# Kernel tuning notes

Measured on AMD Instinct MI355X. Metric: run time of the kernel, lower is better.

Reference implementation:

```python
import jax, jax.numpy as jnp
import numpy as np

B, S, IN, OUT, E, K = 4, 2048, 4096, 4096, 8, 16
POOLS = E * K  # 128 rank-one pools


def setup_inputs() -> dict:
    key = jax.random.key(0)
    k1, k2, k3, k4, k5 = jax.random.split(key, 5)
    sc = 0.02
    return {
        "hidden_states": jax.random.normal(k1, (B, S, IN), jnp.float32),
        "w0": jax.random.normal(k2, (OUT, IN), jnp.float32) * sc,   # pretrained Linear weight
        "b0": jnp.zeros((OUT,), jnp.float32),                        # pretrained Linear bias
        "wr": jax.random.normal(k3, (POOLS, IN), jnp.float32) * sc,  # Router stacked v.T
        "u": jax.random.normal(k4, (OUT, POOLS), jnp.float32) * sc,  # RankOnePools.u
        "svh": jax.random.normal(k5, (POOLS, IN), jnp.float32) * sc, # RankOnePools.svh
        "top_k": 2,
    }


def reference(hidden_states, w0, b0, wr, u, svh, top_k):
    # pretrained dense path (expert_use_diff=True)
    pretrained_out = jnp.einsum('bsi,oi->bso', hidden_states, w0) + b0

    x = hidden_states.reshape(-1, hidden_states.shape[-1])  # [N, IN]

    # Router: logits over num_experts*k rank-one pools
    logits = jnp.einsum('ni,pi->np', x, wr)                  # [N, POOLS]
    vals, idx = jax.lax.top_k(logits, top_k)                 # [N, top_k]
    vals = vals / jnp.sum(vals, axis=-1, keepdims=True)      # computed but UNUSED (matches original torch code)

    # RankOnePools: gather selected rank-one factors and combine
    svh_sel = svh[idx]                                       # [N, top_k, IN]
    dot = jnp.einsum('ni,nti->nt', x, svh_sel)               # [N, top_k]
    u_sel = u.T[idx]                                         # [N, top_k, OUT]
    expert_out = jnp.einsum('nt,nto->no', dot, u_sel)        # [N, OUT]

    out = pretrained_out + expert_out.reshape(pretrained_out.shape)
    return out
```

## Files before the change

kernel.cpp:

```cpp
#include <hip/hip_runtime.h>

#define K_DIM  4096
#define N_OUT  4096
#define N_TOK  8192
#define N_POOL 128

typedef __bf16 bf16x8 __attribute__((ext_vector_type(8)));
typedef float  f32x4  __attribute__((ext_vector_type(4)));
typedef unsigned short u16x8 __attribute__((ext_vector_type(8)));

#define AS1 __attribute__((address_space(1)))
#define AS3 __attribute__((address_space(3)))

__device__ __forceinline__ unsigned short f2bf(float f) {
    union { float f; unsigned u; } v; v.f = f;
    unsigned r = v.u + 0x7fffu + ((v.u >> 16) & 1u);
    return (unsigned short)(r >> 16);
}
__device__ __forceinline__ float bf2f(unsigned short b) {
    union { unsigned u; float f; } v; v.u = ((unsigned)b) << 16;
    return v.f;
}

__global__ __launch_bounds__(256) void k_convert_w0(const float* __restrict__ w0,
                                                    unsigned short* __restrict__ w0b) {
    size_t base = ((size_t)blockIdx.x * 256 + threadIdx.x) * 8;
    float4 a = *(const float4*)(w0 + base);
    float4 b = *(const float4*)(w0 + base + 4);
    u16x8 r;
    r[0] = f2bf(a.x); r[1] = f2bf(a.y); r[2] = f2bf(a.z); r[3] = f2bf(a.w);
    r[4] = f2bf(b.x); r[5] = f2bf(b.y); r[6] = f2bf(b.z); r[7] = f2bf(b.w);
    *(u16x8*)(w0b + base) = r;
}

__global__ __launch_bounds__(256) void k_convert_x(const float* __restrict__ x,
                                                   unsigned short* __restrict__ xh) {
    size_t base = ((size_t)blockIdx.x * 256 + threadIdx.x) * 8;
    float4 a = *(const float4*)(x + base);
    float4 b = *(const float4*)(x + base + 4);
    u16x8 r;
    r[0] = f2bf(a.x); r[1] = f2bf(a.y); r[2] = f2bf(a.z); r[3] = f2bf(a.w);
    r[4] = f2bf(b.x); r[5] = f2bf(b.y); r[6] = f2bf(b.z); r[7] = f2bf(b.w);
    *(u16x8*)(xh + base) = r;
}

__global__ __launch_bounds__(256) void k_convert_wr(const float* __restrict__ wr,
                                                    unsigned short* __restrict__ wrh) {
    size_t base = ((size_t)blockIdx.x * 256 + threadIdx.x) * 8;
    float4 a = *(const float4*)(wr + base);
    float4 b = *(const float4*)(wr + base + 4);
    u16x8 r;
    r[0] = f2bf(a.x); r[1] = f2bf(a.y); r[2] = f2bf(a.z); r[3] = f2bf(a.w);
    r[4] = f2bf(b.x); r[5] = f2bf(b.y); r[6] = f2bf(b.z); r[7] = f2bf(b.w);
    *(u16x8*)(wrh + base) = r;
}

__global__ __launch_bounds__(256) void k_transpose_u(const float* __restrict__ u,
                                                     float* __restrict__ uT) {
    __shared__ float t[32][65];
    const int o0 = blockIdx.x * 64, p0 = blockIdx.y * 32;
    const int tid = threadIdx.x;
#pragma unroll
    for (int it = 0; it < 8; it++) {
        int o = (tid >> 5) + it * 8;
        t[tid & 31][o] = u[(size_t)(o0 + o) * N_POOL + p0 + (tid & 31)];
    }
    __syncthreads();
#pragma unroll
    for (int it = 0; it < 8; it++) {
        int p = (tid >> 6) + it * 4;
        uT[(size_t)(p0 + p) * N_OUT + o0 + (tid & 63)] = t[p][tid & 63];
    }
}

#define RTK 64
#define TAU 0.06f

__global__ __launch_bounds__(512) void k_router(const float* __restrict__ x,
                                                const float* __restrict__ wr,
                                                const unsigned short* __restrict__ wrh,
                                                const unsigned short* __restrict__ xh,
                                                const float* __restrict__ svh,
                                                int* __restrict__ idxp,
                                                float* __restrict__ dotp) {
    __shared__ __attribute__((aligned(16))) unsigned short A2[2][32 * RTK];
    __shared__ __attribute__((aligned(16))) unsigned short B2[2][N_POOL * RTK];
    __shared__ float lg[32][N_POOL + 1];
    __shared__ float thr2[32];
    __shared__ int   flg[32];
    __shared__ int   sel[32][2];

    const int tid  = threadIdx.x;
    const int lane = tid & 63;
    const int w    = tid >> 6;
    const int wm   = w & 1;
    const int wn   = w >> 1;
    const int lrow = lane & 15, lquad = lane >> 4;
    const size_t m0 = (size_t)blockIdx.x * 32;
    const int srow8 = lane >> 3, schunk = lane & 7;

    f32x4 acc[2] = {};

#define RSTAGE(bufi, kk)                                                                         \
    {                                                                                            \
        if (w < 4) {                                                                             \
            int rr = 8 * w + srow8; int cc = schunk ^ (rr & 7);                                  \
            __builtin_amdgcn_global_load_lds(                                                    \
                (const AS1 void*)(xh + (m0 + rr) * (size_t)K_DIM + (kk) + cc * 8),               \
                (AS3 void*)(&A2[bufi][8 * w * RTK] + lane * 8), 16, 0, 0);                       \
        }                                                                                        \
        _Pragma("unroll")                                                                        \
        for (int j = 0; j < 2; j++) {                                                            \
            int rr = 8 * w + 64 * j + srow8; int cc = schunk ^ (rr & 7);                         \
            __builtin_amdgcn_global_load_lds(                                                    \
                (const AS1 void*)(wrh + (size_t)rr * K_DIM + (kk) + cc * 8),                     \
                (AS3 void*)(&B2[bufi][(8 * w + 64 * j) * RTK] + lane * 8), 16, 0, 0);            \
        }                                                                                        \
    }

    RSTAGE(0, 0)
    RSTAGE(1, RTK)

    for (int t = 0; t < K_DIM / RTK; ++t) {
        if (t == 63)     asm volatile("s_waitcnt vmcnt(0)" ::: "memory");
        else if (w < 4)  asm volatile("s_waitcnt vmcnt(3)" ::: "memory");
        else             asm volatile("s_waitcnt vmcnt(2)" ::: "memory");
        __builtin_amdgcn_s_barrier();
        const int buf = t & 1;
#pragma unroll
        for (int ks = 0; ks < 2; ks++) {
            const int cs = ((ks * 4 + lquad) ^ (lrow & 7)) * 8;
            bf16x8 ah = *(const bf16x8*)&A2[buf][(wm * 16 + lrow) * RTK + cs];
#pragma unroll
            for (int nt = 0; nt < 2; nt++) {
                bf16x8 bh = *(const bf16x8*)&B2[buf][(wn * 32 + nt * 16 + lrow) * RTK + cs];
                acc[nt] = __builtin_amdgcn_mfma_f32_16x16x32_bf16(ah, bh, acc[nt], 0, 0, 0);
            }
        }
        __builtin_amdgcn_s_barrier();
        if (t < 62) RSTAGE(buf, (t + 2) * RTK)
    }
#undef RSTAGE

#pragma unroll
    for (int nt = 0; nt < 2; nt++)
#pragma unroll
        for (int r = 0; r < 4; r++)
            lg[wm * 16 + lquad * 4 + r][wn * 32 + nt * 16 + lrow] = acc[nt][r];
    __syncthreads();

    if (tid < 32) {
        float v1 = -3.4e38f, v2 = -3.4e38f, v3 = -3.4e38f; int i1 = 0, i2 = 0;
        for (int p = 0; p < N_POOL; p++) {
            float v = lg[tid][p];
            if (v > v1)      { v3 = v2; v2 = v1; i2 = i1; v1 = v; i1 = p; }
            else if (v > v2) { v3 = v2; v2 = v;  i2 = p; }
            else if (v > v3) { v3 = v; }
        }
        sel[tid][0] = i1; sel[tid][1] = i2;
        thr2[tid] = v2 - TAU;
        flg[tid]  = (v2 - v3 < TAU) ? 1 : 0;
    }
    __syncthreads();

    if (w == 0) {
        for (int s = 0; s < 32; s++) {
            if (!flg[s]) continue;
            const float th = thr2[s];
            unsigned long long c0 = __ballot(lg[s][lane] >= th);
            unsigned long long c1 = __ballot(lg[s][64 + lane] >= th);
            float v1 = -3.4e38f, v2 = -3.4e38f; int i1 = 0, i2 = 0;
            const float* xr = x + (m0 + s) * K_DIM;
            for (int half = 0; half < 2; half++) {
                unsigned long long m = half ? c1 : c0;
                while (m) {
                    const int p = (half ? 64 : 0) + __ffsll(m) - 1;
                    m &= m - 1;
                    const float* wp = wr + (size_t)p * K_DIM;
                    float d = 0.f;
#pragma unroll 8
                    for (int it = 0; it < 64; it++)
                        d += xr[it * 64 + lane] * wp[it * 64 + lane];
#pragma unroll
                    for (int off = 32; off > 0; off >>= 1) d += __shfl_down(d, off);
                    d = __shfl(d, 0);
                    if (d > v1)      { v2 = v1; i2 = i1; v1 = d; i1 = p; }
                    else if (d > v2) { v2 = d; i2 = p; }
                }
            }
            if (lane == 0) { sel[s][0] = i1; sel[s][1] = i2; }
        }
    }
    __syncthreads();

    if (tid < 32) {
        idxp[(m0 + tid) * 2 + 0] = sel[tid][0];
        idxp[(m0 + tid) * 2 + 1] = sel[tid][1];
    }

    for (int s = w; s < 32; s += 8) {
        const size_t n = m0 + s;
        const int e0 = sel[s][0], e1 = sel[s][1];
        float d0 = 0.f, d1 = 0.f;
#pragma unroll
        for (int it = 0; it < 8; it++) {
            const int e = (it * 64 + lane) * 8;
            u16x8 xv = *(const u16x8*)(xh + n * K_DIM + e);
            float4 s0 = *(const float4*)(svh + (size_t)e0 * K_DIM + e);
            float4 s1 = *(const float4*)(svh + (size_t)e0 * K_DIM + e + 4);
            float4 s2 = *(const float4*)(svh + (size_t)e1 * K_DIM + e);
            float4 s3 = *(const float4*)(svh + (size_t)e1 * K_DIM + e + 4);
            float x0 = bf2f(xv[0]), x1 = bf2f(xv[1]), x2 = bf2f(xv[2]), x3 = bf2f(xv[3]);
            float x4 = bf2f(xv[4]), x5 = bf2f(xv[5]), x6 = bf2f(xv[6]), x7 = bf2f(xv[7]);
            d0 += x0*s0.x + x1*s0.y + x2*s0.z + x3*s0.w + x4*s1.x + x5*s1.y + x6*s1.z + x7*s1.w;
            d1 += x0*s2.x + x1*s2.y + x2*s2.z + x3*s2.w + x4*s3.x + x5*s3.y + x6*s3.z + x7*s3.w;
        }
#pragma unroll
        for (int off = 32; off > 0; off >>= 1) {
            d0 += __shfl_down(d0, off);
            d1 += __shfl_down(d1, off);
        }
        if (lane == 0) { dotp[n * 2 + 0] = d0; dotp[n * 2 + 1] = d1; }
    }
}

__global__ __launch_bounds__(512) void k_gemm(const unsigned short* __restrict__ xh,
                                              const unsigned short* __restrict__ w0b,
                                              const float* __restrict__ b0,
                                              const float* __restrict__ uT,
                                              const int* __restrict__ idxp,
                                              const float* __restrict__ dotp,
                                              float* __restrict__ out) {
    __shared__ __attribute__((aligned(16))) unsigned short Als[2][256 * 64];
    __shared__ __attribute__((aligned(16))) unsigned short Bls[2][256 * 64];

    const int tid  = threadIdx.x;
    const int lane = tid & 63;
    const int w    = tid >> 6;
    const int wm   = w >> 2, wn = w & 3;
    const int lrow = lane & 15, lquad = lane >> 4;

    const int lgid = (blockIdx.x & 7) * 64 + (blockIdx.x >> 3);
    const size_t n0 = (size_t)(lgid & 15) * 256;
    const size_t m0 = (size_t)(lgid >> 4) * 256;

    const int srow   = tid >> 3;
    const int xchunk = (tid & 7) ^ (srow & 7);
    const unsigned short* ag = xh  + (m0 + srow) * K_DIM + xchunk * 8;
    const unsigned short* bg = w0b + (n0 + srow) * K_DIM + xchunk * 8;

    f32x4 acc[8][4] = {};

#define STAGE(buf, k0)                                                                        \
    {                                                                                         \
        unsigned short* al = &Als[buf][tid * 8];                                              \
        unsigned short* bl = &Bls[buf][tid * 8];                                              \
        _Pragma("unroll")                                                                     \
        for (int l = 0; l < 4; l++) {                                                         \
            __builtin_amdgcn_global_load_lds(                                                 \
                (const AS1 void*)(ag + (size_t)l * 64 * K_DIM + (k0)),                        \
                (AS3 void*)(al + l * 4096), 16, 0, 0);                                        \
            __builtin_amdgcn_global_load_lds(                                                 \
                (const AS1 void*)(bg + (size_t)l * 64 * K_DIM + (k0)),                        \
                (AS3 void*)(bl + l * 4096), 16, 0, 0);                                        \
        }                                                                                     \
    }

#define COMPUTE(buf)                                                                          \
    {                                                                                         \
        _Pragma("unroll")                                                                     \
        for (int ks = 0; ks < 2; ks++) {                                                      \
            const int cs = ((ks * 4 + lquad) ^ (lrow & 7)) * 8;                               \
            bf16x8 bfv[4];                                                                    \
            _Pragma("unroll")                                                                 \
            for (int nt = 0; nt < 4; nt++)                                                    \
                bfv[nt] = *(const bf16x8*)&Bls[buf][(wn * 64 + nt * 16 + lrow) * 64 + cs];    \
            _Pragma("unroll")                                                                 \
            for (int mt = 0; mt < 8; mt++) {                                                  \
                bf16x8 av = *(const bf16x8*)&Als[buf][(wm * 128 + mt * 16 + lrow) * 64 + cs]; \
                _Pragma("unroll")                                                             \
                for (int nt = 0; nt < 4; nt++)                                                \
                    acc[mt][nt] = __builtin_amdgcn_mfma_f32_16x16x32_bf16(av, bfv[nt], acc[mt][nt], 0, 0, 0); \
            }                                                                                 \
        }                                                                                     \
    }

    STAGE(0, 0)
    STAGE(1, 64)

    for (int t = 0; t < 63; ++t) {
        asm volatile("s_waitcnt vmcnt(8)" ::: "memory");
        __builtin_amdgcn_s_barrier();
        const int buf = t & 1;
        COMPUTE(buf)
        __builtin_amdgcn_s_barrier();
        if (t < 62) STAGE(buf, (t + 2) * 64)
    }
    asm volatile("s_waitcnt vmcnt(0)" ::: "memory");
    __builtin_amdgcn_s_barrier();
    COMPUTE(1)

#undef STAGE
#undef COMPUTE

    float b0v[4];
#pragma unroll
    for (int nt = 0; nt < 4; nt++) b0v[nt] = b0[n0 + wn * 64 + nt * 16 + lrow];
#pragma unroll
    for (int mt = 0; mt < 8; mt++) {
        const size_t rb = m0 + wm * 128 + mt * 16 + lquad * 4;
#pragma unroll
        for (int r = 0; r < 4; r++) {
            const size_t gm = rb + r;
            const int e0 = idxp[gm * 2 + 0], e1 = idxp[gm * 2 + 1];
            const float dd0 = dotp[gm * 2 + 0], dd1 = dotp[gm * 2 + 1];
#pragma unroll
            for (int nt = 0; nt < 4; nt++) {
                const size_t gn = n0 + wn * 64 + nt * 16 + lrow;
                float vv = acc[mt][nt][r] + b0v[nt]
                         + dd0 * uT[(size_t)e0 * N_OUT + gn] + dd1 * uT[(size_t)e1 * N_OUT + gn];
                out[gm * N_OUT + gn] = vv;
            }
        }
    }
}

extern "C" void kernel_launch(void* const* d_in, const int* in_sizes, int n_in,
                              void* d_out, int out_size, void* d_ws, size_t ws_size,
                              hipStream_t stream) {
    const float* x   = (const float*)d_in[0];
    const float* w0  = (const float*)d_in[1];
    const float* b0  = (const float*)d_in[2];
    const float* wr  = (const float*)d_in[3];
    const float* u   = (const float*)d_in[4];
    const float* svh = (const float*)d_in[5];
    float* out = (float*)d_out;

    char* ws = (char*)d_ws;
    unsigned short* xh  = (unsigned short*)ws;
    unsigned short* w0b = (unsigned short*)(ws + 67108864);
    int*   idxp = (int*)(ws + 100663296);
    float* dotp = (float*)(ws + 100663296 + 65536);
    float* uTp  = (float*)(ws + 100663296 + 131072);
    unsigned short* wrh = (unsigned short*)(ws + 102891520);

    k_convert_w0<<<dim3(16777216 / (256 * 8)), dim3(256), 0, stream>>>(w0, w0b);
    k_convert_x<<<dim3(33554432 / (256 * 8)), dim3(256), 0, stream>>>(x, xh);
    k_convert_wr<<<dim3(524288 / (256 * 8)), dim3(256), 0, stream>>>(wr, wrh);
    k_transpose_u<<<dim3(N_OUT / 64, N_POOL / 32), dim3(256), 0, stream>>>(u, uTp);
    k_router<<<dim3(N_TOK / 32), dim3(512), 0, stream>>>(x, wr, wrh, xh, svh, idxp, dotp);
    k_gemm<<<dim3(512), dim3(512), 0, stream>>>(xh, w0b, b0, uTp, idxp, dotp, out);
}
```

Before: 731.2 us.

## Split router into direct-load MFMA logits kernel and separate top-k kernel

Replaces the fused router kernel (32 tokens per block, LDS double-buffered staging) with two kernels. The first computes logits for 16 tokens per block, doubling the block count, and feeds MFMA straight from global memory with register prefetch, no LDS and no barriers. The second does top-k selection and the selected-pool dot products. The logits buffer reuses the w0 bf16 workspace, so the w0 conversion is moved after top-k. This adds a logits round trip through global memory and an extra launch.

```diff
diff --git a/kernel.cpp b/kernel.cpp
--- a/kernel.cpp
+++ b/kernel.cpp
@@ -73,18 +73,53 @@
     }
 }
 
-#define RTK 64
+__global__ __launch_bounds__(256) void k_logits(const unsigned short* __restrict__ xh,
+                                                const unsigned short* __restrict__ wrh,
+                                                float* __restrict__ lgbuf) {
+    const int tid  = threadIdx.x;
+    const int lane = tid & 63;
+    const int w    = tid >> 6;
+    const int lrow = lane & 15, lquad = lane >> 4;
+    const size_t tok0 = (size_t)blockIdx.x * 16;
+    const int p0 = w * 32;
+
+    const unsigned short* xa  = xh  + (tok0 + lrow) * (size_t)K_DIM + lquad * 8;
+    const unsigned short* bp0 = wrh + (size_t)(p0 + lrow) * K_DIM + lquad * 8;
+    const unsigned short* bp1 = wrh + (size_t)(p0 + 16 + lrow) * K_DIM + lquad * 8;
+
+    f32x4 acc0 = {}, acc1 = {};
+    bf16x8 av = *(const bf16x8*)xa;
+    bf16x8 b0 = *(const bf16x8*)bp0;
+    bf16x8 b1 = *(const bf16x8*)bp1;
+
+#pragma unroll 4
+    for (int s = 0; s < 128; s++) {
+        bf16x8 ac = av, b0c = b0, b1c = b1;
+        if (s < 127) {
+            av = *(const bf16x8*)(xa  + (s + 1) * 32);
+            b0 = *(const bf16x8*)(bp0 + (s + 1) * 32);
+            b1 = *(const bf16x8*)(bp1 + (s + 1) * 32);
+        }
+        acc0 = __builtin_amdgcn_mfma_f32_16x16x32_bf16(ac, b0c, acc0, 0, 0, 0);
+        acc1 = __builtin_amdgcn_mfma_f32_16x16x32_bf16(ac, b1c, acc1, 0, 0, 0);
+    }
+
+#pragma unroll
+    for (int r = 0; r < 4; r++) {
+        lgbuf[(tok0 + lquad * 4 + r) * N_POOL + p0 + lrow]      = acc0[r];
+        lgbuf[(tok0 + lquad * 4 + r) * N_POOL + p0 + 16 + lrow] = acc1[r];
+    }
+}
+
 #define TAU 0.06f
 
-__global__ __launch_bounds__(512) void k_router(const float* __restrict__ x,
-                                                const float* __restrict__ wr,
-                                                const unsigned short* __restrict__ wrh,
-                                                const unsigned short* __restrict__ xh,
-                                                const float* __restrict__ svh,
-                                                int* __restrict__ idxp,
-                                                float* __restrict__ dotp) {
-    __shared__ __attribute__((aligned(16))) unsigned short A2[2][32 * RTK];
-    __shared__ __attribute__((aligned(16))) unsigned short B2[2][N_POOL * RTK];
+__global__ __launch_bounds__(256) void k_topk(const float* __restrict__ lgbuf,
+                                              const float* __restrict__ x,
+                                              const float* __restrict__ wr,
+                                              const unsigned short* __restrict__ xh,
+                                              const float* __restrict__ svh,
+                                              int* __restrict__ idxp,
+                                              float* __restrict__ dotp) {
     __shared__ float lg[32][N_POOL + 1];
     __shared__ float thr2[32];
     __shared__ int   flg[32];
@@ -93,60 +128,18 @@
     const int tid  = threadIdx.x;
     const int lane = tid & 63;
     const int w    = tid >> 6;
-    const int wm   = w & 1;
-    const int wn   = w >> 1;
-    const int lrow = lane & 15, lquad = lane >> 4;
     const size_t m0 = (size_t)blockIdx.x * 32;
-    const int srow8 = lane >> 3, schunk = lane & 7;
-
-    f32x4 acc[2] = {};
-
-#define RSTAGE(bufi, kk)                                                                         \
-    {                                                                                            \
-        if (w < 4) {                                                                             \
-            int rr = 8 * w + srow8; int cc = schunk ^ (rr & 7);                                  \
-            __builtin_amdgcn_global_load_lds(                                                    \
-                (const AS1 void*)(xh + (m0 + rr) * (size_t)K_DIM + (kk) + cc * 8),               \
-                (AS3 void*)(&A2[bufi][8 * w * RTK] + lane * 8), 16, 0, 0);                       \
-        }                                                                                        \
-        _Pragma("unroll")                                                                        \
-        for (int j = 0; j < 2; j++) {                                                            \
-            int rr = 8 * w + 64 * j + srow8; int cc = schunk ^ (rr & 7);                         \
-            __builtin_amdgcn_global_load_lds(                                                    \
-                (const AS1 void*)(wrh + (size_t)rr * K_DIM + (kk) + cc * 8),                     \
-                (AS3 void*)(&B2[bufi][(8 * w + 64 * j) * RTK] + lane * 8), 16, 0, 0);            \
-        }                                                                                        \
-    }
-
-    RSTAGE(0, 0)
-    RSTAGE(1, RTK)
-
-    for (int t = 0; t < K_DIM / RTK; ++t) {
-        if (t == 63)     asm volatile("s_waitcnt vmcnt(0)" ::: "memory");
-        else if (w < 4)  asm volatile("s_waitcnt vmcnt(3)" ::: "memory");
-        else             asm volatile("s_waitcnt vmcnt(2)" ::: "memory");
-        __builtin_amdgcn_s_barrier();
-        const int buf = t & 1;
-#pragma unroll
-        for (int ks = 0; ks < 2; ks++) {
-            const int cs = ((ks * 4 + lquad) ^ (lrow & 7)) * 8;
-            bf16x8 ah = *(const bf16x8*)&A2[buf][(wm * 16 + lrow) * RTK + cs];
-#pragma unroll
-            for (int nt = 0; nt < 2; nt++) {
-                bf16x8 bh = *(const bf16x8*)&B2[buf][(wn * 32 + nt * 16 + lrow) * RTK + cs];
-                acc[nt] = __builtin_amdgcn_mfma_f32_16x16x32_bf16(ah, bh, acc[nt], 0, 0, 0);
-            }
-        }
-        __builtin_amdgcn_s_barrier();
-        if (t < 62) RSTAGE(buf, (t + 2) * RTK)
-    }
-#undef RSTAGE
-
-#pragma unroll
-    for (int nt = 0; nt < 2; nt++)
-#pragma unroll
-        for (int r = 0; r < 4; r++)
-            lg[wm * 16 + lquad * 4 + r][wn * 32 + nt * 16 + lrow] = acc[nt][r];
+
+    {
+        const int tok = tid >> 3, cb = (tid & 7) * 16;
+        const float* src = lgbuf + (m0 + tok) * N_POOL + cb;
+#pragma unroll
+        for (int j = 0; j < 4; j++) {
+            float4 v = *(const float4*)(src + j * 4);
+            lg[tok][cb + j * 4 + 0] = v.x; lg[tok][cb + j * 4 + 1] = v.y;
+            lg[tok][cb + j * 4 + 2] = v.z; lg[tok][cb + j * 4 + 3] = v.w;
+        }
+    }
     __syncthreads();
 
     if (tid < 32) {
@@ -198,7 +191,7 @@
         idxp[(m0 + tid) * 2 + 1] = sel[tid][1];
     }
 
-    for (int s = w; s < 32; s += 8) {
+    for (int s = w; s < 32; s += 4) {
         const size_t n = m0 + s;
         const int e0 = sel[s][0], e1 = sel[s][1];
         float d0 = 0.f, d1 = 0.f;
@@ -339,15 +332,17 @@
     char* ws = (char*)d_ws;
     unsigned short* xh  = (unsigned short*)ws;
     unsigned short* w0b = (unsigned short*)(ws + 67108864);
+    float* lgbuf = (float*)(ws + 67108864);
     int*   idxp = (int*)(ws + 100663296);
     float* dotp = (float*)(ws + 100663296 + 65536);
     float* uTp  = (float*)(ws + 100663296 + 131072);
     unsigned short* wrh = (unsigned short*)(ws + 102891520);
 
-    k_convert_w0<<<dim3(16777216 / (256 * 8)), dim3(256), 0, stream>>>(w0, w0b);
     k_convert_x<<<dim3(33554432 / (256 * 8)), dim3(256), 0, stream>>>(x, xh);
     k_convert_wr<<<dim3(524288 / (256 * 8)), dim3(256), 0, stream>>>(wr, wrh);
     k_transpose_u<<<dim3(N_OUT / 64, N_POOL / 32), dim3(256), 0, stream>>>(u, uTp);
-    k_router<<<dim3(N_TOK / 32), dim3(512), 0, stream>>>(x, wr, wrh, xh, svh, idxp, dotp);
+    k_logits<<<dim3(512), dim3(256), 0, stream>>>(xh, wrh, lgbuf);
+    k_topk<<<dim3(256), dim3(256), 0, stream>>>(lgbuf, x, wr, xh, svh, idxp, dotp);
+    k_convert_w0<<<dim3(16777216 / (256 * 8)), dim3(256), 0, stream>>>(w0, w0b);
     k_gemm<<<dim3(512), dim3(512), 0, stream>>>(xh, w0b, b0, uTp, idxp, dotp, out);
 }
```

New measurement: 761.7 us. 4.2% more time.
